# Kernel tuning notes

Measured on AMD Instinct MI355X. Metric: run time of the kernel, lower is better.

The kernel has to match this reference:

```python
import jax, jax.numpy as jnp
import numpy as np

FILTERS = 64
NBITS = 4
NUE = 4
NSPU = 2
NST = NUE * NSPU           # 8 streams total
OUT_CH = NST * NBITS       # 32 output channels
NBS, NANT = 1, 16
CIN = NBS * NANT * 2 + NBS * NANT * NUE * NSPU * 2 + NUE * NSPU + 1  # 297


def hard_sigmoid(x):
    # Keras ConvLSTM2D default recurrent_activation
    return jnp.clip(0.2 * x + 0.5, 0.0, 1.0)


def conv2d(x, w):
    # x: [N,H,W,C], w: [kh,kw,Cin,Cout], SAME padding
    return jax.lax.conv_general_dilated(x, w, (1, 1), 'SAME',
                                        dimension_numbers=('NHWC', 'HWIO', 'NHWC'))


def convlstm2d(x, Wx, Wh, b):
    """Keras ConvLSTM2D (return_sequences=True), gate order i,f,c,o.
    x: [B,T,H,W,Cin] -> [B,T,H,W,F].
    Input-to-hidden convs are precomputed for all timesteps at once;
    only the cheap hidden-to-hidden conv is inside the scan."""
    B, T, H, W, Cin = x.shape
    F = Wh.shape[2]
    xz = conv2d(x.reshape(B * T, H, W, Cin), Wx).reshape(B, T, H, W, 4 * F) + b
    xz = jnp.moveaxis(xz, 1, 0)  # [T,B,H,W,4F]
    h0 = jnp.zeros((B, H, W, F), x.dtype)

    def step(carry, z_in):
        h, c = carry
        z = z_in + conv2d(h, Wh)
        zi, zf, zg, zo = jnp.split(z, 4, axis=-1)
        i = hard_sigmoid(zi)
        f = hard_sigmoid(zf)
        g = jnp.tanh(zg)
        o = hard_sigmoid(zo)
        c = f * c + i * g
        h = o * jnp.tanh(c)
        return (h, c), h

    _, hs = jax.lax.scan(step, (h0, h0), xz)
    return jnp.moveaxis(hs, 0, 1)  # [B,T,H,W,F]


def _lstm_params(key, cin, f, scale=0.05):
    k1, k2, k3 = jax.random.split(key, 3)
    Wx = jax.random.normal(k1, (3, 3, cin, 4 * f), jnp.float32) * scale
    Wh = jax.random.normal(k2, (3, 3, f, 4 * f), jnp.float32) * scale
    b = jax.random.normal(k3, (4 * f,), jnp.float32) * scale
    return Wx, Wh, b


def setup_inputs() -> dict:
    key = jax.random.key(0)
    ks = jax.random.split(key, 10)
    B, T, W = 2, 14, 1536
    inp = {
        'y_ri': jax.random.normal(ks[0], (B, NBS, NANT, T, W, 2), jnp.float32),
        'h_ri': jax.random.normal(ks[1], (B, NBS, NANT, NUE, NSPU, T, W, 2), jnp.float32),
        'err_var': jax.random.uniform(ks[2], (1, 1, 1, NUE, NSPU, T, W), jnp.float32),
        'no': jax.random.uniform(ks[3], (1,), jnp.float32),
    }
    inp['Wx_in'], inp['Wh_in'], inp['b_in'] = _lstm_params(ks[4], CIN, FILTERS)
    inp['Wx_r0'], inp['Wh_r0'], inp['b_r0'] = _lstm_params(ks[5], FILTERS, FILTERS)
    inp['Wx_r1'], inp['Wh_r1'], inp['b_r1'] = _lstm_params(ks[6], FILTERS, FILTERS)
    inp['Wx_out'], inp['Wh_out'], inp['b_out'] = _lstm_params(ks[7], FILTERS, OUT_CH)
    return inp


def _forward(y_ri, h_ri, err_var, no,
             Wx_in, Wh_in, b_in,
             Wx_r0, Wh_r0, b_r0,
             Wx_r1, Wh_r1, b_r1,
             Wx_out, Wh_out, b_out):
    B, nbs, nant, T, W, _ = y_ri.shape
    # y: [B,nbs,nant,T,W,2] -> [B,T,W,nbs*nant*2]
    y_feats = jnp.transpose(y_ri, (0, 3, 4, 1, 2, 5)).reshape(B, T, W, -1)
    # h: [B,nbs,nant,ue,spu,T,W,2] -> [B,T,W,nbs*nant*ue*spu*2]
    h_feats = jnp.transpose(h_ri, (0, 5, 6, 1, 2, 3, 4, 7)).reshape(B, T, W, -1)
    # err_var: [1,1,1,ue,spu,T,W] -> [B,T,W,ue*spu]
    ev = jnp.transpose(err_var[0, 0, 0], (2, 3, 0, 1)).reshape(1, T, W, NUE * NSPU)
    err_feats = jnp.broadcast_to(ev, (B, T, W, NUE * NSPU))
    no_feat = jnp.broadcast_to(no.reshape(1, 1, 1, 1), (B, T, W, 1))
    z = jnp.concatenate([y_feats, h_feats, err_feats, no_feat], axis=-1)
    z = z[:, :, :, None, :]  # [B,T,W,1,C]

    z = convlstm2d(z, Wx_in, Wh_in, b_in)
    # residual blocks (in_ch == filters, so identity skip)
    z = convlstm2d(z, Wx_r0, Wh_r0, b_r0) + z
    z = convlstm2d(z, Wx_r1, Wh_r1, b_r1) + z
    z = convlstm2d(z, Wx_out, Wh_out, b_out)

    z = z[:, :, :, 0, :]  # [B,T,W,OUT_CH]
    N = T * W
    z = z.reshape(B, N, NUE, NSPU, NBITS)
    z = jnp.transpose(z, (0, 2, 3, 1, 4))
    return z.reshape(B, NUE, NSPU, N * NBITS)


def reference(y_ri, h_ri, err_var, no,
              Wx_in, Wh_in, b_in,
              Wx_r0, Wh_r0, b_r0,
              Wx_r1, Wh_r1, b_r1,
              Wx_out, Wh_out, b_out):
    return _forward(y_ri, h_ri, err_var, no,
                    Wx_in, Wh_in, b_in,
                    Wx_r0, Wh_r0, b_r0,
                    Wx_r1, Wh_r1, b_r1,
                    Wx_out, Wh_out, b_out)
```

## Files before the change

kernel.cpp:

```cpp
#include <hip/hip_runtime.h>
#include <hip/hip_bf16.h>


#define BB   2
#define TT   14
#define LL   1536
#define LL2  1538
#define CINR 297
#define CP_IN 320
#define NSTRIP 96
#define NBLK  (BB * NSTRIP)
#define WIN  48

typedef __attribute__((ext_vector_type(8))) short short8;
typedef __attribute__((ext_vector_type(4))) float floatx4;

__device__ __forceinline__ void lds_barrier() {
    asm volatile("s_waitcnt lgkmcnt(0)" ::: "memory");
    __builtin_amdgcn_s_barrier();
}

static constexpr size_t U_WBIN_HI  = 0;
static constexpr size_t U_WBIN_LO  = 245760;
static constexpr size_t U_WBR0_HI  = 491520;
static constexpr size_t U_WBR0_LO  = 540672;
static constexpr size_t U_WBR1_HI  = 589824;
static constexpr size_t U_WBR1_LO  = 638976;
static constexpr size_t U_WBOUT_HI = 688128;
static constexpr size_t U_WBOUT_LO = 712704;
static constexpr size_t U_WHTIN    = 737280;
static constexpr size_t U_WHTR0    = 786432;
static constexpr size_t U_WHTR1    = 835584;
static constexpr size_t U_WHTOUT   = 884736;
static constexpr size_t OFF_BIN   = 448512;
static constexpr size_t OFF_BR0   = 448768;
static constexpr size_t OFF_BR1   = 449024;
static constexpr size_t OFF_BOUT  = 449280;
static constexpr size_t OFF_Z0HI  = 458752;
static constexpr size_t SZ_Z0PL   = 6890240;
static constexpr size_t OFF_Z0LO  = OFF_Z0HI + SZ_Z0PL;
static constexpr size_t OFF_XZ    = OFF_Z0LO + SZ_Z0PL;
static constexpr size_t SZ_XZ     = (size_t)BB*TT*LL*256;
static constexpr size_t OFF_SEQ   = OFF_Z0HI;
static constexpr size_t OFF_SEQHI = OFF_SEQ + (size_t)BB*TT*LL2*64;
static constexpr size_t OFF_SEQLO = OFF_SEQHI + (size_t)BB*TT*LL2*32;

__device__ __forceinline__ float hsig(float x) {
    return fminf(fmaxf(0.2f * x + 0.5f, 0.0f), 1.0f);
}
__device__ __forceinline__ float ftanh(float x) {
    float e = __expf(2.0f * x);
    return 1.0f - 2.0f / (e + 1.0f);
}
__device__ __forceinline__ unsigned short f2bf(float x) {
    unsigned int u = __builtin_bit_cast(unsigned int, x);
    u += 0x7fffu + ((u >> 16) & 1u);
    return (unsigned short)(u >> 16);
}
__device__ __forceinline__ float bf2f(unsigned short h) {
    unsigned int u = ((unsigned int)h) << 16;
    return __builtin_bit_cast(float, u);
}

__global__ __launch_bounds__(256)
void zero_pads_kernel(unsigned short* __restrict__ z0hi,
                      unsigned short* __restrict__ z0lo)
{
    int idx = blockIdx.x * 256 + threadIdx.x;
    const int NZ = BB * TT * 2 * CP_IN;
    if (idx < NZ) {
        int c = idx % CP_IN, r2 = idx / CP_IN;
        int p = r2 >> 1, e = r2 & 1;
        long long off = ((long long)p * LL2 + (e ? (LL2 - 1) : 0)) * CP_IN + c;
        z0hi[off] = 0; z0lo[off] = 0;
    }
}

__global__ __launch_bounds__(256)
void zero_seq_pads_kernel(unsigned short* __restrict__ seqhb,
                          unsigned short* __restrict__ seqlb)
{
    int idx = blockIdx.x * 256 + threadIdx.x;
    const int NS = BB * TT * 2 * 64;
    if (idx < NS) {
        int c = idx % 64, r2 = idx / 64;
        int p = r2 >> 1, e = r2 & 1;
        long long off = ((long long)p * LL2 + (e ? (LL2 - 1) : 0)) * 64 + c;
        seqhb[off] = 0; seqlb[off] = 0;
    }
}

__global__ __launch_bounds__(256)
void prep_weights_kernel(const float* wx_in, const float* wh_in, const float* b_in,
                         const float* wx_r0, const float* wh_r0, const float* b_r0,
                         const float* wx_r1, const float* wh_r1, const float* b_r1,
                         const float* wx_out, const float* wh_out, const float* b_out,
                         float* __restrict__ ws)
{
    int idx = blockIdx.x * 256 + threadIdx.x;
    unsigned short* u = (unsigned short*)ws;
    if (idx < 245760) {
        int j = idx & 7, lane = (idx >> 3) & 63, frag = idx >> 9;
        int g = frag & 15, rest = frag >> 4;
        int kh = rest % 3, cc = rest / 3;
        int mm = lane & 15, quad = lane >> 4;
        int n = g * 16 + mm;
        int ci = cc * 32 + quad * 8 + j;
        float v = 0.0f;
        if (ci < CINR)
            v = wx_in[((size_t)(kh * 3 + 1) * CINR + ci) * 256 + (n & 3) * 64 + (n >> 2)];
        unsigned short hi = f2bf(v);
        u[U_WBIN_HI + idx] = hi;
        u[U_WBIN_LO + idx] = f2bf(v - bf2f(hi));
        return;
    }
    idx -= 245760;
    if (idx < 49152) {
        int j = idx & 7, lane = (idx >> 3) & 63, frag = idx >> 9;
        int g = frag & 15, rest = frag >> 4;
        int kh = rest % 3, cc = rest / 3;
        int mm = lane & 15, quad = lane >> 4;
        int n = g * 16 + mm;
        int ci = cc * 32 + quad * 8 + j;
        float v = wx_r0[((size_t)(kh * 3 + 1) * 64 + ci) * 256 + (n & 3) * 64 + (n >> 2)];
        unsigned short hi = f2bf(v);
        u[U_WBR0_HI + idx] = hi;
        u[U_WBR0_LO + idx] = f2bf(v - bf2f(hi));
        return;
    }
    idx -= 49152;
    if (idx < 49152) {
        int j = idx & 7, lane = (idx >> 3) & 63, frag = idx >> 9;
        int g = frag & 15, rest = frag >> 4;
        int kh = rest % 3, cc = rest / 3;
        int mm = lane & 15, quad = lane >> 4;
        int n = g * 16 + mm;
        int ci = cc * 32 + quad * 8 + j;
        float v = wx_r1[((size_t)(kh * 3 + 1) * 64 + ci) * 256 + (n & 3) * 64 + (n >> 2)];
        unsigned short hi = f2bf(v);
        u[U_WBR1_HI + idx] = hi;
        u[U_WBR1_LO + idx] = f2bf(v - bf2f(hi));
        return;
    }
    idx -= 49152;
    if (idx < 24576) {
        int j = idx & 7, lane = (idx >> 3) & 63, frag = idx >> 9;
        int g = frag & 7, rest = frag >> 3;
        int kh = rest % 3, cc = rest / 3;
        int mm = lane & 15, quad = lane >> 4;
        int n = g * 16 + mm;
        int ci = cc * 32 + quad * 8 + j;
        float v = wx_out[((size_t)(kh * 3 + 1) * 64 + ci) * 128 + (n & 3) * 32 + (n >> 2)];
        unsigned short hi = f2bf(v);
        u[U_WBOUT_HI + idx] = hi;
        u[U_WBOUT_LO + idx] = f2bf(v - bf2f(hi));
        return;
    }
    idx -= 24576;
    if (idx < 49152) {
        int n = idx / 192, k = idx % 192, kh = k >> 6, ci = k & 63;
        u[U_WHTIN + idx] = f2bf(wh_in[((size_t)(kh * 3 + 1) * 64 + ci) * 256 + n]);
        return;
    }
    idx -= 49152;
    if (idx < 49152) {
        int n = idx / 192, k = idx % 192, kh = k >> 6, ci = k & 63;
        u[U_WHTR0 + idx] = f2bf(wh_r0[((size_t)(kh * 3 + 1) * 64 + ci) * 256 + n]);
        return;
    }
    idx -= 49152;
    if (idx < 49152) {
        int n = idx / 192, k = idx % 192, kh = k >> 6, ci = k & 63;
        u[U_WHTR1 + idx] = f2bf(wh_r1[((size_t)(kh * 3 + 1) * 64 + ci) * 256 + n]);
        return;
    }
    idx -= 49152;
    if (idx < 12288) {
        int n = idx / 96, k = idx % 96, kh = k / 32, ci = k % 32;
        u[U_WHTOUT + idx] = f2bf(wh_out[((size_t)(kh * 3 + 1) * 32 + ci) * 128 + n]);
        return;
    }
    idx -= 12288;
    if (idx < 256) { int f = idx >> 2, g = idx & 3; ws[OFF_BIN + idx] = b_in[g * 64 + f]; return; }
    idx -= 256;
    if (idx < 256) { int f = idx >> 2, g = idx & 3; ws[OFF_BR0 + idx] = b_r0[g * 64 + f]; return; }
    idx -= 256;
    if (idx < 256) { int f = idx >> 2, g = idx & 3; ws[OFF_BR1 + idx] = b_r1[g * 64 + f]; return; }
    idx -= 256;
    if (idx < 128) { int f = idx >> 2, g = idx & 3; ws[OFF_BOUT + idx] = b_out[g * 32 + f]; return; }
}

__global__ __launch_bounds__(256)
void build_features_kernel(const float* __restrict__ y,
                           const float* __restrict__ h,
                           const float* __restrict__ ev,
                           const float* __restrict__ no,
                           unsigned short* __restrict__ z0hi,
                           unsigned short* __restrict__ z0lo)
{
    long long idx = (long long)blockIdx.x * 256 + threadIdx.x;
    const long long total = (long long)BB * TT * LL * CP_IN;
    if (idx >= total) return;
    int c = (int)(idx % CP_IN);
    long long rest = idx / CP_IN;
    int l = (int)(rest % LL); rest /= LL;
    int t = (int)(rest % TT);
    int b = (int)(rest / TT);
    float v = 0.0f;
    if (c < 32) {
        int na = c >> 1, ri = c & 1;
        v = y[((((long long)b * 16 + na) * TT + t) * LL + l) * 2 + ri];
    } else if (c < 288) {
        int q = c - 32;
        int ri = q & 1, nspu = (q >> 1) & 1, nue = (q >> 2) & 3, na = q >> 4;
        v = h[((((((long long)b * 16 + na) * 4 + nue) * 2 + nspu) * TT + t) * LL + l) * 2 + ri];
    } else if (c < 296) {
        int q = c - 288; int nspu = q & 1, nue = q >> 1;
        v = ev[(((long long)(nue * 2 + nspu) * TT + t) * LL) + l];
    } else if (c == 296) {
        v = no[0];
    }
    const long long widx = (((long long)(b * TT + t)) * LL2 + (l + 1)) * CP_IN + c;
    unsigned short hi = f2bf(v);
    z0hi[widx] = hi;
    z0lo[widx] = f2bf(v - bf2f(hi));
}

template <int CP>
__global__ __launch_bounds__(256)
void xz_gemm_mfma_kernel(const unsigned short* __restrict__ Ahi,
                         const unsigned short* __restrict__ Alo,
                         const unsigned short* __restrict__ Bphi,
                         const unsigned short* __restrict__ Bplo,
                         const float* __restrict__ bias,
                         float* __restrict__ out, int Ncol)
{
    constexpr int NCm = CP / 64;
    __shared__ unsigned short AsHi[66 * 72], AsLo[66 * 72];
    const int tid  = threadIdx.x;
    const int lane = tid & 63;
    const int wv   = tid >> 6;
    const int m    = lane & 15;
    const int quad = lane >> 4;
    const int bt   = blockIdx.y;
    const int l0   = blockIdx.x * 64;
    const int n0   = blockIdx.z * 128;
    const int NG   = Ncol >> 4;
    const int gBase = (n0 >> 4) + wv;

    const int r0s = tid >> 3,        c0 = (tid & 7) * 8;
    const int r1s = (tid + 256) >> 3, c1 = (tid & 7) * 8;
    const int r2s = 64 + (tid >> 3),  c2 = (tid & 7) * 8;
    const long long aG0 = ((long long)bt * LL2 + l0 + r0s) * CP + c0;
    const long long aG1 = ((long long)bt * LL2 + l0 + r1s) * CP + c1;
    const long long aG2 = ((long long)bt * LL2 + l0 + r2s) * CP + c2;

    short8 g0h, g0l, g1h, g1l, g2h = (short8)0, g2l = (short8)0;

    g0h = *reinterpret_cast<const short8*>(&Ahi[aG0]);
    g0l = *reinterpret_cast<const short8*>(&Alo[aG0]);
    g1h = *reinterpret_cast<const short8*>(&Ahi[aG1]);
    g1l = *reinterpret_cast<const short8*>(&Alo[aG1]);
    if (tid < 16) {
        g2h = *reinterpret_cast<const short8*>(&Ahi[aG2]);
        g2l = *reinterpret_cast<const short8*>(&Alo[aG2]);
    }

    floatx4 acc[4][2];
#pragma unroll
    for (int i = 0; i < 4; i++)
#pragma unroll
        for (int j = 0; j < 2; j++) acc[i][j] = (floatx4){0.f, 0.f, 0.f, 0.f};

#pragma unroll 1
    for (int mc = 0; mc < NCm; ++mc) {
        lds_barrier();
        *reinterpret_cast<short8*>(&AsHi[r0s * 72 + c0]) = g0h;
        *reinterpret_cast<short8*>(&AsLo[r0s * 72 + c0]) = g0l;
        *reinterpret_cast<short8*>(&AsHi[r1s * 72 + c1]) = g1h;
        *reinterpret_cast<short8*>(&AsLo[r1s * 72 + c1]) = g1l;
        if (tid < 16) {
            *reinterpret_cast<short8*>(&AsHi[r2s * 72 + c2]) = g2h;
            *reinterpret_cast<short8*>(&AsLo[r2s * 72 + c2]) = g2l;
        }
        lds_barrier();
        if (mc + 1 < NCm) {
            const int co = (mc + 1) * 64;
            g0h = *reinterpret_cast<const short8*>(&Ahi[aG0 + co]);
            g0l = *reinterpret_cast<const short8*>(&Alo[aG0 + co]);
            g1h = *reinterpret_cast<const short8*>(&Ahi[aG1 + co]);
            g1l = *reinterpret_cast<const short8*>(&Alo[aG1 + co]);
            if (tid < 16) {
                g2h = *reinterpret_cast<const short8*>(&Ahi[aG2 + co]);
                g2l = *reinterpret_cast<const short8*>(&Alo[aG2 + co]);
            }
        }
#pragma unroll
        for (int sub = 0; sub < 2; ++sub) {
            const int cc = mc * 2 + sub;
            short8 bh[3][2], bl[3][2];
#pragma unroll
            for (int kh = 0; kh < 3; ++kh)
#pragma unroll
                for (int nt = 0; nt < 2; ++nt) {
                    const size_t off =
                        ((size_t)((cc * 3 + kh) * NG + gBase + nt * 4)) * 512 + lane * 8;
                    bh[kh][nt] = *reinterpret_cast<const short8*>(&Bphi[off]);
                    bl[kh][nt] = *reinterpret_cast<const short8*>(&Bplo[off]);
                }
#pragma unroll
            for (int kh = 0; kh < 3; ++kh) {
#pragma unroll
                for (int mt = 0; mt < 4; ++mt) {
                    const int aofs = (mt * 16 + m + kh) * 72 + sub * 32 + quad * 8;
                    const short8 ah = *reinterpret_cast<const short8*>(&AsHi[aofs]);
                    const short8 al = *reinterpret_cast<const short8*>(&AsLo[aofs]);
                    acc[mt][0] = __builtin_amdgcn_mfma_f32_16x16x32_bf16(al, bh[kh][0], acc[mt][0], 0, 0, 0);
                    acc[mt][0] = __builtin_amdgcn_mfma_f32_16x16x32_bf16(ah, bl[kh][0], acc[mt][0], 0, 0, 0);
                    acc[mt][0] = __builtin_amdgcn_mfma_f32_16x16x32_bf16(ah, bh[kh][0], acc[mt][0], 0, 0, 0);
                    acc[mt][1] = __builtin_amdgcn_mfma_f32_16x16x32_bf16(al, bh[kh][1], acc[mt][1], 0, 0, 0);
                    acc[mt][1] = __builtin_amdgcn_mfma_f32_16x16x32_bf16(ah, bl[kh][1], acc[mt][1], 0, 0, 0);
                    acc[mt][1] = __builtin_amdgcn_mfma_f32_16x16x32_bf16(ah, bh[kh][1], acc[mt][1], 0, 0, 0);
                }
            }
        }
    }

#pragma unroll
    for (int nt = 0; nt < 2; ++nt) {
        const int col = n0 + nt * 64 + wv * 16 + m;
        const float bv = bias[col];
#pragma unroll
        for (int mt = 0; mt < 4; ++mt) {
#pragma unroll
            for (int reg = 0; reg < 4; ++reg) {
                int l = l0 + mt * 16 + quad * 4 + reg;
                out[((size_t)bt * LL + l) * Ncol + col] = acc[mt][nt][reg] + bv;
            }
        }
    }
}

template <int F_, bool RESID, bool OUTW, bool WRSEQ>
__global__ __launch_bounds__(64 * (F_ / 16))
void lstm_scan_kernel(const float* __restrict__ xz,
                      const unsigned short* __restrict__ WhT,
                      float* seq,
                      unsigned short* __restrict__ seqhb,
                      unsigned short* __restrict__ seqlb,
                      float* __restrict__ dout)
{
    constexpr int NW = F_ / 16;
    constexpr int NT = 64 * NW;
    constexpr int K  = 3 * F_;
    constexpr int KS = K / 32;
    constexpr int KH = KS / 3;
    constexpr int HP = F_ + 8;
    __shared__ unsigned short Hs[2][(WIN + 2) * HP];

    const int tid  = threadIdx.x;
    const int lane = tid & 63;
    const int wv   = tid >> 6;
    const int m    = lane & 15;
    const int quad = lane >> 4;
    const int blk  = (blockIdx.x & 7) * (NBLK / 8) + (blockIdx.x >> 3);
    const int b    = blk / NSTRIP;
    const int o0   = (blk % NSTRIP) * 16;
    const int f    = wv * 16 + m;

    short8 bfr[4][KS];
#pragma unroll
    for (int g = 0; g < 4; g++)
#pragma unroll
        for (int ks = 0; ks < KS; ks++) {
            const int n  = g * F_ + f;
            const int k0 = ks * 32 + quad * 8;
            bfr[g][ks] = *reinterpret_cast<const short8*>(&WhT[(size_t)n * K + k0]);
        }

    for (int idx = tid; idx < (WIN + 2) * HP; idx += NT) {
        Hs[0][idx] = 0; Hs[1][idx] = 0;
    }
    __syncthreads();

    float c[3][4];
#pragma unroll
    for (int i = 0; i < 3; i++)
#pragma unroll
        for (int j = 0; j < 4; j++) c[i][j] = 0.0f;

    int cur = 0;
    for (int t = 0; t < TT; ++t) {
        const size_t btL  = ((size_t)b * TT + t) * LL;
        const size_t btLP = ((size_t)b * TT + t) * LL2;

        float4 xzv[3][4];
        float  rsv[4];
#pragma unroll
        for (int mt = 0; mt < 3; ++mt)
#pragma unroll
            for (int reg = 0; reg < 4; ++reg) {
                const int w = mt * 16 + quad * 4 + reg;
                const int l = o0 - 16 + w;
                float4 v = make_float4(0.f, 0.f, 0.f, 0.f);
                if (l >= 0 && l < LL && w >= t && w < WIN - t)
                    v = *reinterpret_cast<const float4*>(
                        &xz[(btL + l) * (size_t)(4 * F_) + f * 4]);
                xzv[mt][reg] = v;
            }
        if (RESID) {
#pragma unroll
            for (int reg = 0; reg < 4; ++reg) {
                const int l = o0 + quad * 4 + reg;
                rsv[reg] = seq[(btLP + 1 + l) * F_ + f];
            }
        }

        const int nxt = cur ^ 1;
#pragma unroll
        for (int mt = 0; mt < 3; ++mt) {
            floatx4 zi = {0.f, 0.f, 0.f, 0.f};
            floatx4 zf = {0.f, 0.f, 0.f, 0.f};
            floatx4 zg = {0.f, 0.f, 0.f, 0.f};
            floatx4 zo = {0.f, 0.f, 0.f, 0.f};
            if (t > 0) {
#pragma unroll
                for (int kh = 0; kh < 3; kh++) {
#pragma unroll
                    for (int hf = 0; hf < KH; hf++) {
                        const short8 af = *reinterpret_cast<const short8*>(
                            &Hs[cur][(mt * 16 + m + kh) * HP + hf * 32 + quad * 8]);
                        const int ks = kh * KH + hf;
                        zi = __builtin_amdgcn_mfma_f32_16x16x32_bf16(af, bfr[0][ks], zi, 0, 0, 0);
                        zf = __builtin_amdgcn_mfma_f32_16x16x32_bf16(af, bfr[1][ks], zf, 0, 0, 0);
                        zg = __builtin_amdgcn_mfma_f32_16x16x32_bf16(af, bfr[2][ks], zg, 0, 0, 0);
                        zo = __builtin_amdgcn_mfma_f32_16x16x32_bf16(af, bfr[3][ks], zo, 0, 0, 0);
                    }
                }
            }
#pragma unroll
            for (int reg = 0; reg < 4; ++reg) {
                const int w = mt * 16 + quad * 4 + reg;
                const int l = o0 - 16 + w;
                const bool valid = (l >= 0 && l < LL);
                const float4 z4 = xzv[mt][reg];
                const float ig = hsig(z4.x + zi[reg]);
                const float fg = hsig(z4.y + zf[reg]);
                const float gg = ftanh(z4.z + zg[reg]);
                const float og = hsig(z4.w + zo[reg]);
                float cn = fg * c[mt][reg] + ig * gg;
                float hn = og * ftanh(cn);
                if (!valid) { cn = 0.0f; hn = 0.0f; }
                c[mt][reg] = cn;
                Hs[nxt][(1 + w) * HP + f] = f2bf(hn);
                if (w >= 16 && w < 32) {
                    if (OUTW) {
                        const int ue = f >> 3, spu = (f >> 2) & 1, bit = f & 3;
                        const size_t n = (size_t)t * LL + l;
                        dout[(((size_t)b * 4 + ue) * 2 + spu) * ((size_t)TT * LL * 4)
                             + n * 4 + bit] = hn;
                    } else {
                        float v = hn;
                        if (RESID) v += rsv[reg];
                        if (WRSEQ) seq[(btLP + 1 + l) * F_ + f] = v;
                        const unsigned short hi2 = f2bf(v);
                        seqhb[(btLP + 1 + l) * F_ + f] = hi2;
                        seqlb[(btLP + 1 + l) * F_ + f] = f2bf(v - bf2f(hi2));
                    }
                }
            }
        }
        lds_barrier();
        cur = nxt;
    }
}

extern "C" void kernel_launch(void* const* d_in, const int* in_sizes, int n_in,
                              void* d_out, int out_size, void* d_ws, size_t ws_size,
                              hipStream_t stream)
{
    (void)in_sizes; (void)n_in; (void)out_size; (void)ws_size;
    const float* y_ri   = (const float*)d_in[0];
    const float* h_ri   = (const float*)d_in[1];
    const float* evar   = (const float*)d_in[2];
    const float* no     = (const float*)d_in[3];
    const float* wx_in  = (const float*)d_in[4];
    const float* wh_in  = (const float*)d_in[5];
    const float* b_in   = (const float*)d_in[6];
    const float* wx_r0  = (const float*)d_in[7];
    const float* wh_r0  = (const float*)d_in[8];
    const float* b_r0   = (const float*)d_in[9];
    const float* wx_r1  = (const float*)d_in[10];
    const float* wh_r1  = (const float*)d_in[11];
    const float* b_r1   = (const float*)d_in[12];
    const float* wx_out = (const float*)d_in[13];
    const float* wh_out = (const float*)d_in[14];
    const float* b_out  = (const float*)d_in[15];

    float* ws = (float*)d_ws;
    unsigned short* wu = (unsigned short*)d_ws;
    float* dout = (float*)d_out;

    unsigned short* z0hi = (unsigned short*)(ws + OFF_Z0HI);
    unsigned short* z0lo = (unsigned short*)(ws + OFF_Z0LO);
    float* xz    = ws + OFF_XZ;
    float* seq   = ws + OFF_SEQ;
    unsigned short* seqhb = (unsigned short*)(ws + OFF_SEQHI);
    unsigned short* seqlb = (unsigned short*)(ws + OFF_SEQLO);

    zero_pads_kernel<<<70, 256, 0, stream>>>(z0hi, z0lo);
    prep_weights_kernel<<<2068, 256, 0, stream>>>(
        wx_in, wh_in, b_in, wx_r0, wh_r0, b_r0,
        wx_r1, wh_r1, b_r1, wx_out, wh_out, b_out, ws);
    {
        long long total = (long long)BB * TT * LL * CP_IN;
        int blocks = (int)((total + 255) / 256);
        build_features_kernel<<<blocks, 256, 0, stream>>>(
            y_ri, h_ri, evar, no, z0hi, z0lo);
    }

    const dim3 gIn(LL / 64, BB * TT, 2);
    const dim3 gO (LL / 64, BB * TT, 1);

    xz_gemm_mfma_kernel<CP_IN><<<gIn, 256, 0, stream>>>(
        z0hi, z0lo, wu + U_WBIN_HI, wu + U_WBIN_LO, ws + OFF_BIN, xz, 256);
    zero_seq_pads_kernel<<<14, 256, 0, stream>>>(seqhb, seqlb);
    lstm_scan_kernel<64, false, false, true><<<NBLK, 256, 0, stream>>>(
        xz, wu + U_WHTIN, seq, seqhb, seqlb, nullptr);

    xz_gemm_mfma_kernel<64><<<gIn, 256, 0, stream>>>(
        seqhb, seqlb, wu + U_WBR0_HI, wu + U_WBR0_LO, ws + OFF_BR0, xz, 256);
    lstm_scan_kernel<64, true, false, true><<<NBLK, 256, 0, stream>>>(
        xz, wu + U_WHTR0, seq, seqhb, seqlb, nullptr);

    xz_gemm_mfma_kernel<64><<<gIn, 256, 0, stream>>>(
        seqhb, seqlb, wu + U_WBR1_HI, wu + U_WBR1_LO, ws + OFF_BR1, xz, 256);
    lstm_scan_kernel<64, true, false, false><<<NBLK, 256, 0, stream>>>(
        xz, wu + U_WHTR1, seq, seqhb, seqlb, nullptr);

    xz_gemm_mfma_kernel<64><<<gO, 256, 0, stream>>>(
        seqhb, seqlb, wu + U_WBOUT_HI, wu + U_WBOUT_LO, ws + OFF_BOUT, xz, 128);
    lstm_scan_kernel<32, false, true, false><<<NBLK, 128, 0, stream>>>(
        xz, wu + U_WHTOUT, nullptr, nullptr, nullptr, dout);
}
```

Before: 486.2 us.

## Fuse input-to-hidden GEMM into residual ConvLSTM scan kernels

For the two residual ConvLSTM layers, the separate xz GEMM kernel and its fp32 xz buffer round-trip are replaced by a fused scan kernel. It computes the input conv per timestep from bf16 hi/lo sequence tiles staged and double-buffered in LDS, then runs the recurrent conv and gate math in the same block. Input and output sequence buffers are ping-ponged to avoid read/write hazards. The cost is extra MFMA work and global weight loads on the serial per-timestep critical path, plus more LDS per block, which may lower occupancy.

```diff
diff --git a/kernel.cpp b/kernel.cpp
--- a/kernel.cpp
+++ b/kernel.cpp
@@ -44,6 +44,8 @@
 static constexpr size_t OFF_SEQ   = OFF_Z0HI;
 static constexpr size_t OFF_SEQHI = OFF_SEQ + (size_t)BB*TT*LL2*64;
 static constexpr size_t OFF_SEQLO = OFF_SEQHI + (size_t)BB*TT*LL2*32;
+static constexpr size_t OFF_SQBHI = OFF_XZ;
+static constexpr size_t OFF_SQBLO = OFF_XZ + (size_t)BB*TT*LL2*32;
 
 __device__ __forceinline__ float hsig(float x) {
     return fminf(fmaxf(0.2f * x + 0.5f, 0.0f), 1.0f);
@@ -77,8 +79,8 @@
 }
 
 __global__ __launch_bounds__(256)
-void zero_seq_pads_kernel(unsigned short* __restrict__ seqhb,
-                          unsigned short* __restrict__ seqlb)
+void zero_seq_pads_kernel(unsigned short* __restrict__ hb,
+                          unsigned short* __restrict__ lb)
 {
     int idx = blockIdx.x * 256 + threadIdx.x;
     const int NS = BB * TT * 2 * 64;
@@ -86,7 +88,7 @@
         int c = idx % 64, r2 = idx / 64;
         int p = r2 >> 1, e = r2 & 1;
         long long off = ((long long)p * LL2 + (e ? (LL2 - 1) : 0)) * 64 + c;
-        seqhb[off] = 0; seqlb[off] = 0;
+        hb[off] = 0; lb[off] = 0;
     }
 }
 
@@ -345,7 +347,7 @@
 __global__ __launch_bounds__(64 * (F_ / 16))
 void lstm_scan_kernel(const float* __restrict__ xz,
                       const unsigned short* __restrict__ WhT,
-                      float* seq,
+                      float* __restrict__ seq,
                       unsigned short* __restrict__ seqhb,
                       unsigned short* __restrict__ seqlb,
                       float* __restrict__ dout)
@@ -475,6 +477,192 @@
     }
 }
 
+template <bool WRSEQ>
+__global__ __launch_bounds__(256)
+void fused_scan_kernel(const unsigned short* __restrict__ inHb,
+                       const unsigned short* __restrict__ inLb,
+                       const unsigned short* __restrict__ Bphi,
+                       const unsigned short* __restrict__ Bplo,
+                       const float* __restrict__ bias,
+                       const unsigned short* __restrict__ WhT,
+                       float* __restrict__ seq,
+                       unsigned short* __restrict__ outHb,
+                       unsigned short* __restrict__ outLb)
+{
+    constexpr int K  = 192, KS = 6, KH = 2;
+    constexpr int HP = 72, XP = 72;
+    constexpr int XR = WIN + 2;
+    __shared__ unsigned short Hs[2][XR * HP];
+    __shared__ unsigned short XsH[2][XR * XP], XsL[2][XR * XP];
+
+    const int tid  = threadIdx.x;
+    const int lane = tid & 63;
+    const int wv   = tid >> 6;
+    const int m    = lane & 15;
+    const int quad = lane >> 4;
+    const int blk  = (blockIdx.x & 7) * (NBLK / 8) + (blockIdx.x >> 3);
+    const int b    = blk / NSTRIP;
+    const int o0   = (blk % NSTRIP) * 16;
+    const int f    = wv * 16 + m;
+
+    short8 bfr[4][KS];
+#pragma unroll
+    for (int g = 0; g < 4; g++)
+#pragma unroll
+        for (int ks = 0; ks < KS; ks++)
+            bfr[g][ks] = *reinterpret_cast<const short8*>(
+                &WhT[(size_t)(g * 64 + f) * K + ks * 32 + quad * 8]);
+
+    const int bpl = (wv * 4 + (m >> 2)) * 512 + (quad * 16 + (m & 3) * 4) * 8;
+    float bv[4];
+#pragma unroll
+    for (int g = 0; g < 4; g++) bv[g] = bias[f * 4 + g];
+
+    const int ch0x = tid >> 3,         ch0c = (tid & 7) * 8;
+    const int ch1x = (tid + 256) >> 3, ch1c = (tid & 7) * 8;
+    const int gl0  = o0 - 16 + ch0x;
+    const int gl1  = o0 - 16 + ch1x;
+    const bool v0  = (gl0 >= 0 && gl0 < LL2);
+    const bool v1  = (tid < 144) && (gl1 >= 0 && gl1 < LL2);
+
+    for (int idx = tid; idx < XR * HP; idx += 256) {
+        Hs[0][idx] = 0; Hs[1][idx] = 0;
+    }
+    {
+        const size_t base = (size_t)b * TT * LL2;
+        short8 h0 = (short8)0, l0 = (short8)0, h1 = (short8)0, l1 = (short8)0;
+        if (v0) {
+            h0 = *reinterpret_cast<const short8*>(&inHb[(base + gl0) * 64 + ch0c]);
+            l0 = *reinterpret_cast<const short8*>(&inLb[(base + gl0) * 64 + ch0c]);
+        }
+        if (v1) {
+            h1 = *reinterpret_cast<const short8*>(&inHb[(base + gl1) * 64 + ch1c]);
+            l1 = *reinterpret_cast<const short8*>(&inLb[(base + gl1) * 64 + ch1c]);
+        }
+        *reinterpret_cast<short8*>(&XsH[0][ch0x * XP + ch0c]) = h0;
+        *reinterpret_cast<short8*>(&XsL[0][ch0x * XP + ch0c]) = l0;
+        if (tid < 144) {
+            *reinterpret_cast<short8*>(&XsH[0][ch1x * XP + ch1c]) = h1;
+            *reinterpret_cast<short8*>(&XsL[0][ch1x * XP + ch1c]) = l1;
+        }
+    }
+    __syncthreads();
+
+    float c[3][4];
+#pragma unroll
+    for (int i = 0; i < 3; i++)
+#pragma unroll
+        for (int j = 0; j < 4; j++) c[i][j] = 0.0f;
+
+    int cur = 0;
+#pragma unroll 1
+    for (int t = 0; t < TT; ++t) {
+        const size_t btLP = ((size_t)b * TT + t) * LL2;
+        const int nxt = cur ^ 1;
+
+        short8 sh0 = (short8)0, sl0 = (short8)0, sh1 = (short8)0, sl1 = (short8)0;
+        if (t + 1 < TT) {
+            const size_t basen = ((size_t)b * TT + (t + 1)) * LL2;
+            if (v0) {
+                sh0 = *reinterpret_cast<const short8*>(&inHb[(basen + gl0) * 64 + ch0c]);
+                sl0 = *reinterpret_cast<const short8*>(&inLb[(basen + gl0) * 64 + ch0c]);
+            }
+            if (v1) {
+                sh1 = *reinterpret_cast<const short8*>(&inHb[(basen + gl1) * 64 + ch1c]);
+                sl1 = *reinterpret_cast<const short8*>(&inLb[(basen + gl1) * 64 + ch1c]);
+            }
+        }
+        float rsv[4];
+#pragma unroll
+        for (int reg = 0; reg < 4; ++reg)
+            rsv[reg] = seq[(btLP + 1 + o0 + quad * 4 + reg) * 64 + f];
+
+        floatx4 acc[3][4];
+#pragma unroll
+        for (int mt = 0; mt < 3; ++mt)
+#pragma unroll
+            for (int g = 0; g < 4; ++g)
+                acc[mt][g] = (floatx4){bv[g], bv[g], bv[g], bv[g]};
+
+#pragma unroll
+        for (int cc = 0; cc < 2; ++cc) {
+#pragma unroll
+            for (int kh = 0; kh < 3; ++kh) {
+                const int fb = ((cc * 3 + kh) * 16) * 512 + bpl;
+                short8 bh[4], bl[4];
+#pragma unroll
+                for (int g = 0; g < 4; ++g) {
+                    bh[g] = *reinterpret_cast<const short8*>(&Bphi[fb + g * 8]);
+                    bl[g] = *reinterpret_cast<const short8*>(&Bplo[fb + g * 8]);
+                }
+#pragma unroll
+                for (int mt = 0; mt < 3; ++mt) {
+                    const int ax = (mt * 16 + m + kh) * XP + cc * 32 + quad * 8;
+                    const short8 ah = *reinterpret_cast<const short8*>(&XsH[cur][ax]);
+                    const short8 al = *reinterpret_cast<const short8*>(&XsL[cur][ax]);
+#pragma unroll
+                    for (int g = 0; g < 4; ++g) {
+                        acc[mt][g] = __builtin_amdgcn_mfma_f32_16x16x32_bf16(al, bh[g], acc[mt][g], 0, 0, 0);
+                        acc[mt][g] = __builtin_amdgcn_mfma_f32_16x16x32_bf16(ah, bl[g], acc[mt][g], 0, 0, 0);
+                        acc[mt][g] = __builtin_amdgcn_mfma_f32_16x16x32_bf16(ah, bh[g], acc[mt][g], 0, 0, 0);
+                    }
+                }
+            }
+        }
+        if (t > 0) {
+#pragma unroll
+            for (int mt = 0; mt < 3; ++mt)
+#pragma unroll
+                for (int kh = 0; kh < 3; ++kh)
+#pragma unroll
+                    for (int hf = 0; hf < KH; ++hf) {
+                        const short8 af = *reinterpret_cast<const short8*>(
+                            &Hs[cur][(mt * 16 + m + kh) * HP + hf * 32 + quad * 8]);
+                        const int ks = kh * KH + hf;
+#pragma unroll
+                        for (int g = 0; g < 4; ++g)
+                            acc[mt][g] = __builtin_amdgcn_mfma_f32_16x16x32_bf16(
+                                af, bfr[g][ks], acc[mt][g], 0, 0, 0);
+                    }
+        }
+#pragma unroll
+        for (int mt = 0; mt < 3; ++mt) {
+#pragma unroll
+            for (int reg = 0; reg < 4; ++reg) {
+                const int w = mt * 16 + quad * 4 + reg;
+                const int l = o0 - 16 + w;
+                const bool valid = (l >= 0 && l < LL);
+                const float ig = hsig(acc[mt][0][reg]);
+                const float fg = hsig(acc[mt][1][reg]);
+                const float gg = ftanh(acc[mt][2][reg]);
+                const float og = hsig(acc[mt][3][reg]);
+                float cn = fg * c[mt][reg] + ig * gg;
+                float hn = og * ftanh(cn);
+                if (!valid) { cn = 0.0f; hn = 0.0f; }
+                c[mt][reg] = cn;
+                Hs[nxt][(1 + w) * HP + f] = f2bf(hn);
+                if (w >= 16 && w < 32) {
+                    float v = hn + rsv[reg];
+                    if (WRSEQ) seq[(btLP + 1 + l) * 64 + f] = v;
+                    const unsigned short hi2 = f2bf(v);
+                    outHb[(btLP + 1 + l) * 64 + f] = hi2;
+                    outLb[(btLP + 1 + l) * 64 + f] = f2bf(v - bf2f(hi2));
+                }
+            }
+        }
+        if (t + 1 < TT) {
+            *reinterpret_cast<short8*>(&XsH[nxt][ch0x * XP + ch0c]) = sh0;
+            *reinterpret_cast<short8*>(&XsL[nxt][ch0x * XP + ch0c]) = sl0;
+            if (tid < 144) {
+                *reinterpret_cast<short8*>(&XsH[nxt][ch1x * XP + ch1c]) = sh1;
+                *reinterpret_cast<short8*>(&XsL[nxt][ch1x * XP + ch1c]) = sl1;
+            }
+        }
+        lds_barrier();
+        cur = nxt;
+    }
+}
+
 extern "C" void kernel_launch(void* const* d_in, const int* in_sizes, int n_in,
                               void* d_out, int out_size, void* d_ws, size_t ws_size,
                               hipStream_t stream)
@@ -505,8 +693,10 @@
     unsigned short* z0lo = (unsigned short*)(ws + OFF_Z0LO);
     float* xz    = ws + OFF_XZ;
     float* seq   = ws + OFF_SEQ;
-    unsigned short* seqhb = (unsigned short*)(ws + OFF_SEQHI);
-    unsigned short* seqlb = (unsigned short*)(ws + OFF_SEQLO);
+    unsigned short* seqAh = (unsigned short*)(ws + OFF_SEQHI);
+    unsigned short* seqAl = (unsigned short*)(ws + OFF_SEQLO);
+    unsigned short* seqBh = (unsigned short*)(ws + OFF_SQBHI);
+    unsigned short* seqBl = (unsigned short*)(ws + OFF_SQBLO);
 
     zero_pads_kernel<<<70, 256, 0, stream>>>(z0hi, z0lo);
     prep_weights_kernel<<<2068, 256, 0, stream>>>(
@@ -524,22 +714,22 @@
 
     xz_gemm_mfma_kernel<CP_IN><<<gIn, 256, 0, stream>>>(
         z0hi, z0lo, wu + U_WBIN_HI, wu + U_WBIN_LO, ws + OFF_BIN, xz, 256);
-    zero_seq_pads_kernel<<<14, 256, 0, stream>>>(seqhb, seqlb);
+    zero_seq_pads_kernel<<<14, 256, 0, stream>>>(seqAh, seqAl);
     lstm_scan_kernel<64, false, false, true><<<NBLK, 256, 0, stream>>>(
-        xz, wu + U_WHTIN, seq, seqhb, seqlb, nullptr);
-
-    xz_gemm_mfma_kernel<64><<<gIn, 256, 0, stream>>>(
-        seqhb, seqlb, wu + U_WBR0_HI, wu + U_WBR0_LO, ws + OFF_BR0, xz, 256);
-    lstm_scan_kernel<64, true, false, true><<<NBLK, 256, 0, stream>>>(
-        xz, wu + U_WHTR0, seq, seqhb, seqlb, nullptr);
-
-    xz_gemm_mfma_kernel<64><<<gIn, 256, 0, stream>>>(
-        seqhb, seqlb, wu + U_WBR1_HI, wu + U_WBR1_LO, ws + OFF_BR1, xz, 256);
-    lstm_scan_kernel<64, true, false, false><<<NBLK, 256, 0, stream>>>(
-        xz, wu + U_WHTR1, seq, seqhb, seqlb, nullptr);
+        xz, wu + U_WHTIN, seq, seqAh, seqAl, nullptr);
+
+    zero_seq_pads_kernel<<<14, 256, 0, stream>>>(seqBh, seqBl);
+
+    fused_scan_kernel<true><<<NBLK, 256, 0, stream>>>(
+        seqAh, seqAl, wu + U_WBR0_HI, wu + U_WBR0_LO, ws + OFF_BR0,
+        wu + U_WHTR0, seq, seqBh, seqBl);
+
+    fused_scan_kernel<false><<<NBLK, 256, 0, stream>>>(
+        seqBh, seqBl, wu + U_WBR1_HI, wu + U_WBR1_LO, ws + OFF_BR1,
+        wu + U_WHTR1, seq, seqAh, seqAl);
 
     xz_gemm_mfma_kernel<64><<<gO, 256, 0, stream>>>(
-        seqhb, seqlb, wu + U_WBOUT_HI, wu + U_WBOUT_LO, ws + OFF_BOUT, xz, 128);
+        seqAh, seqAl, wu + U_WBOUT_HI, wu + U_WBOUT_LO, ws + OFF_BOUT, xz, 128);
     lstm_scan_kernel<32, false, true, false><<<NBLK, 128, 0, stream>>>(
         xz, wu + U_WHTOUT, nullptr, nullptr, nullptr, dout);
 }
```

Result: no change. 489.1 us (+0.6%).
